# Performance work log

Hardware: AMD Instinct MI355X
Metric: run time of the kernel (lower is better)

## Reference

```python
import jax, jax.numpy as jnp
import numpy as np

D = 4096      # hidden_size
H = 32        # num_attention_heads
DH = 128      # head_dim
DR = 64       # rope_head_dim (rotated suffix of head_dim)
G = 4         # o_groups
QLR = 1536    # q_lora_rank
OLR = 512     # o_lora_rank
WIN = 2048    # window_size
EPS = 1e-6    # norm_eps
THETA = 10000.0


def rms_norm(x, g):
    return x * jax.lax.rsqrt(jnp.mean(x * x, axis=-1, keepdims=True) + EPS) * g


def rope_interleave(x, cos, sin):
    # interleaved (non-neox) rotary: pairs are adjacent even/odd lanes
    x0, x1 = x[..., 0::2], x[..., 1::2]
    r0 = x0 * cos - x1 * sin
    r1 = x0 * sin + x1 * cos
    return jnp.stack([r0, r1], axis=-1).reshape(x.shape)


def setup_inputs() -> dict:
    ks = jax.random.split(jax.random.key(0), 9)
    B, S = 1, 2048
    return {
        "hidden_states": jax.random.normal(ks[0], (B, S, D), jnp.float32),
        "positions": jnp.arange(S, dtype=jnp.int64),
        "wq_a": jax.random.normal(ks[1], (QLR, D), jnp.float32) * 0.02,
        "q_norm_g": jnp.ones((QLR,), jnp.float32),
        "wq_b": jax.random.normal(ks[2], (H * DH, QLR), jnp.float32) * 0.02,
        "wkv": jax.random.normal(ks[3], (DH, D), jnp.float32) * 0.02,
        "kv_norm_g": jnp.ones((DH,), jnp.float32),
        "wo_a": jax.random.normal(ks[4], (G, OLR, (H * DH) // G), jnp.float32) * 0.02,
        "wo_b": jax.random.normal(ks[5], (D, G * OLR), jnp.float32) * 0.02,
        "attn_sink": jax.random.normal(ks[6], (H,), jnp.float32),
    }


def reference(hidden_states, positions, wq_a, q_norm_g, wq_b, wkv, kv_norm_g, wo_a, wo_b, attn_sink):
    B, S, _ = hidden_states.shape
    # low-rank Q path: wq_a -> RMSNorm -> wq_b -> [B,S,H,DH]
    qr = rms_norm(hidden_states @ wq_a.T, q_norm_g)
    q = (qr @ wq_b.T).reshape(B, S, H, DH)
    # shared latent KV (single head_dim vector, MLA/MQA style): wkv -> RMSNorm
    kv = rms_norm(hidden_states @ wkv.T, kv_norm_g)  # [B,S,DH]
    # rotary tables (interleave mode)
    inv_freq = 1.0 / (THETA ** (jnp.arange(0, DR, 2, dtype=jnp.float32) / DR))
    ang = positions.astype(jnp.float32)[:, None] * inv_freq  # [S, DR/2]
    cos, sin = jnp.cos(ang), jnp.sin(ang)
    # rotate last DR dims of q and k
    q = jnp.concatenate(
        [q[..., : DH - DR], rope_interleave(q[..., DH - DR :], cos[None, :, None, :], sin[None, :, None, :])], -1)
    k = jnp.concatenate(
        [kv[..., : DH - DR], rope_interleave(kv[..., DH - DR :], cos[None, :, :], sin[None, :, :])], -1)
    # windowed causal attention with learned per-head sink logit
    scores = jnp.einsum("bshd,btd->bhst", q, k) * (DH ** -0.5)  # [B,H,S,S]
    i = jnp.arange(S)[:, None]
    j = jnp.arange(S)[None, :]
    mask = (j <= i) & ((i - j) < WIN)
    scores = jnp.where(mask[None, None], scores, jnp.finfo(scores.dtype).min)
    sink = jnp.broadcast_to(attn_sink[None, :, None, None], (B, H, S, 1))
    probs = jax.nn.softmax(jnp.concatenate([scores, sink], axis=-1), axis=-1)[..., :S]
    # value = shared normalized latent (pre-rope)
    out = jnp.einsum("bhst,btd->bshd", probs, kv)  # [B,S,H,DH]
    # grouped low-rank output projection: wo_a per group, then wo_b
    out = out.reshape(B, S, G, (H * DH) // G)
    low = jnp.einsum("bsgd,gkd->bsgk", out, wo_a).reshape(B, S, G * OLR)
    return low @ wo_b.T
```

## Files before the change

kernel.cpp:

```cpp
#include <hip/hip_runtime.h>

typedef unsigned short u16;
typedef __bf16 bf16x8 __attribute__((ext_vector_type(8)));
typedef float  f32x4  __attribute__((ext_vector_type(4)));

#define EPSF 1e-6f

__device__ __forceinline__ u16 f2b(float f) {
  unsigned u = __float_as_uint(f);
  u += 0x7fffu + ((u >> 16) & 1u);
  return (u16)(u >> 16);
}
__device__ __forceinline__ float b2f(u16 u) { return __uint_as_float(((unsigned)u) << 16); }
__device__ __forceinline__ u16 f2bh(float f) { return __builtin_bit_cast(u16, (__bf16)f); }

__device__ __forceinline__ void dma16(const u16* g, u16* l) {
  __builtin_amdgcn_global_load_lds(
      (const __attribute__((address_space(1))) unsigned int*)g,
      (__attribute__((address_space(3))) unsigned int*)l, 16, 0, 0);
}

__global__ void dsv4_cvt(const float* __restrict__ hidden, const float* __restrict__ wq_a,
                         const float* __restrict__ wq_b, const float* __restrict__ wkv,
                         const float* __restrict__ wo_a, const float* __restrict__ wo_b,
                         u16* hb, u16* qab, u16* qbb, u16* kvb, u16* oab, u16* obb)
{
  long c = (long)blockIdx.x * 256 + threadIdx.x;
  const float* s; u16* d; long off;
  if      (c < 1048576) { s = hidden; d = hb;  off = c; }
  else if (c < 1835008) { s = wq_a;   d = qab; off = c - 1048576; }
  else if (c < 2621440) { s = wq_b;   d = qbb; off = c - 1835008; }
  else if (c < 2686976) { s = wkv;    d = kvb; off = c - 2621440; }
  else if (c < 2949120) { s = wo_a;   d = oab; off = c - 2686976; }
  else                  { s = wo_b;   d = obb; off = c - 2949120; }
  const float* p = s + off * 8;
  float4 f0 = *(const float4*)p;
  float4 f1 = *(const float4*)(p + 4);
  union { u16 h[8]; int4 v; } u;
  u.h[0] = f2b(f0.x); u.h[1] = f2b(f0.y); u.h[2] = f2b(f0.z); u.h[3] = f2b(f0.w);
  u.h[4] = f2b(f1.x); u.h[5] = f2b(f1.y); u.h[6] = f2b(f1.z); u.h[7] = f2b(f1.w);
  *(int4*)(d + off * 8) = u.v;
}

template<int BM, bool C_F32>
__global__ __launch_bounds__(256, 2)
void dsv4_gemm(const u16* __restrict__ A, int lda, long sAz,
               const u16* __restrict__ B, int ldb, long sBz,
               void* __restrict__ Cv, int ldc, long sCz,
               int K, int splitTile,
               const u16* __restrict__ Baux, void* __restrict__ Caux, int ldcAux)
{
  constexpr int AI = (BM * 4) / 256;
  constexpr int NJ = (BM == 128) ? 4 : 2;
  __shared__ __align__(16) u16 As[BM * 32];
  __shared__ __align__(16) u16 Bs[128 * 32];

  const int tid   = threadIdx.x;
  const int lane  = tid & 63;
  const int q     = lane >> 4;
  const int l16   = lane & 15;
  const int wid   = tid >> 6;
  const int wbase = tid & 192;

  int n0 = blockIdx.x * 128;
  const int m0 = blockIdx.y * BM;
  void* Cp = Cv;
  if ((int)blockIdx.x >= splitTile) {
    B = Baux; Cp = Caux; ldc = ldcAux;
    n0 = ((int)blockIdx.x - splitTile) * 128;
  }
  A += (long)blockIdx.z * sAz;
  B += (long)blockIdx.z * sBz;

  const u16* gA[AI]; u16* lA[AI];
#pragma unroll
  for (int j = 0; j < AI; j++) {
    int L = j * 256 + tid, row = L >> 2, c = (L & 3) ^ ((row >> 1) & 3);
    gA[j] = A + (long)(m0 + row) * lda + c * 8;
    lA[j] = As + (j * 256 + wbase) * 8;
  }
  const u16* gB[2]; u16* lB[2];
#pragma unroll
  for (int j = 0; j < 2; j++) {
    int L = j * 256 + tid, row = L >> 2, c = (L & 3) ^ ((row >> 1) & 3);
    gB[j] = B + (long)(n0 + row) * ldb + c * 8;
    lB[j] = Bs + (j * 256 + wbase) * 8;
  }

  f32x4 acc[4][NJ];
#pragma unroll
  for (int i = 0; i < 4; i++)
#pragma unroll
    for (int j = 0; j < NJ; j++) { f32x4 z = {0.f, 0.f, 0.f, 0.f}; acc[i][j] = z; }

  const int wm = (BM == 128) ? (wid >> 1) * 64 : 0;
  const int wn = (BM == 128) ? (wid & 1) * 64 : wid * 32;

  for (int k0 = 0; k0 < K; k0 += 32) {
    __syncthreads();
#pragma unroll
    for (int j = 0; j < AI; j++) dma16(gA[j] + k0, lA[j]);
#pragma unroll
    for (int j = 0; j < 2; j++)  dma16(gB[j] + k0, lB[j]);
    asm volatile("s_waitcnt vmcnt(0)" ::: "memory");
    __syncthreads();

    bf16x8 af[4], bg[NJ];
#pragma unroll
    for (int i = 0; i < 4; i++) {
      int row = wm + i * 16 + l16;
      af[i] = *(const bf16x8*)&As[row * 32 + ((q ^ ((row >> 1) & 3)) << 3)];
    }
#pragma unroll
    for (int j = 0; j < NJ; j++) {
      int row = wn + j * 16 + l16;
      bg[j] = *(const bf16x8*)&Bs[row * 32 + ((q ^ ((row >> 1) & 3)) << 3)];
    }
#pragma unroll
    for (int i = 0; i < 4; i++)
#pragma unroll
      for (int j = 0; j < NJ; j++)
        acc[i][j] = __builtin_amdgcn_mfma_f32_16x16x32_bf16(af[i], bg[j], acc[i][j], 0, 0, 0);
  }

#pragma unroll
  for (int i = 0; i < 4; i++)
#pragma unroll
    for (int j = 0; j < NJ; j++)
#pragma unroll
      for (int rr = 0; rr < 4; rr++) {
        long row = m0 + wm + i * 16 + q * 4 + rr;
        int  col = n0 + wn + j * 16 + l16;
        if (C_F32)
          ((float*)Cp)[row * ldc + col + (long)blockIdx.z * sCz] = acc[i][j][rr];
        else
          ((u16*)Cp)[row * ldc + col + (long)blockIdx.z * sCz] = f2b(acc[i][j][rr]);
      }
}

__global__ void dsv4_rmsnorm(const u16* __restrict__ X, const float* __restrict__ g,
                             u16* __restrict__ Y, int W, float invW)
{
  __shared__ float wsum[4];
  const int row = blockIdx.x;
  const u16* x = X + (long)row * W;
  u16* y = Y + (long)row * W;
  float ss = 0.f;
  for (int i = threadIdx.x; i < W; i += 256) { float v = b2f(x[i]); ss += v * v; }
#pragma unroll
  for (int o = 32; o > 0; o >>= 1) ss += __shfl_xor(ss, o);
  const int wid = threadIdx.x >> 6;
  if ((threadIdx.x & 63) == 0) wsum[wid] = ss;
  __syncthreads();
  float tot = wsum[0] + wsum[1] + wsum[2] + wsum[3];
  float scale = rsqrtf(tot * invW + EPSF);
  for (int i = threadIdx.x; i < W; i += 256)
    y[i] = f2b(b2f(x[i]) * scale * g[i]);
}

__global__ void dsv4_kv_finalize(const u16* __restrict__ KVp, const float* __restrict__ g,
                                 u16* __restrict__ Kout, u16* __restrict__ VTout)
{
  const int wid  = threadIdx.x >> 6;
  const int lane = threadIdx.x & 63;
  const int row  = blockIdx.x * 4 + wid;
  const u16* x = KVp + (long)row * 128;
  float x0 = b2f(x[2 * lane]);
  float x1 = b2f(x[2 * lane + 1]);
  float ss = x0 * x0 + x1 * x1;
#pragma unroll
  for (int o = 32; o > 0; o >>= 1) ss += __shfl_xor(ss, o);
  float scale = rsqrtf(ss * (1.f / 128.f) + EPSF);
  float v0 = x0 * scale * g[2 * lane];
  float v1 = x1 * scale * g[2 * lane + 1];
  VTout[(long)(2 * lane) * 2048 + row]     = f2b(v0);
  VTout[(long)(2 * lane + 1) * 2048 + row] = f2b(v1);
  float k0 = v0, k1 = v1;
  if (lane >= 32) {
    int i = lane - 32;
    float invf = powf(10000.f, -(float)i * (1.f / 32.f));
    float sn, cc;
    sincosf((float)row * invf, &sn, &cc);
    k0 = v0 * cc - v1 * sn;
    k1 = v0 * sn + v1 * cc;
  }
  Kout[(long)row * 128 + 2 * lane]     = f2b(k0);
  Kout[(long)row * 128 + 2 * lane + 1] = f2b(k1);
}

__device__ __forceinline__ void attn_step(
    const bf16x8* qf, bool diag, const u16* __restrict__ KsB,
    const u16* __restrict__ VsB, u16* __restrict__ PsW,
    int w, int qd, int l16, int swz, float* m, float* negm, float* l, f32x4* o)
{
  const float scl2 = 0.12754245006257017f;
  const float THRU = 62.0f;
  f32x4 st[4];
#pragma unroll
  for (int i = 0; i < 4; i++) { f32x4 z = {0.f, 0.f, 0.f, 0.f}; st[i] = z; }

  __builtin_amdgcn_s_setprio(1);
#pragma unroll
  for (int ks = 0; ks < 4; ks++) {
#pragma unroll
    for (int nt = 0; nt < 4; nt++) {
      int row = nt * 16 + l16;
      bf16x8 bk = *(const bf16x8*)&KsB[row * 128 + ((((ks << 2) + qd) ^ swz) << 3)];
      st[nt] = __builtin_amdgcn_mfma_f32_16x16x32_bf16(qf[ks], bk, st[nt], 0, 0, 0);
    }
  }
  __builtin_amdgcn_s_setprio(0);

  if (diag) {
#pragma unroll
    for (int nt = 0; nt < 4; nt++)
#pragma unroll
      for (int rr = 0; rr < 4; rr++)
        if ((nt * 16 + l16) > (w * 16 + qd * 4 + rr)) st[nt][rr] = -3.0e38f;
  }

  float tm[4];
  bool need = false;
#pragma unroll
  for (int rr = 0; rr < 4; rr++) {
    float t = fmaxf(fmaxf(st[0][rr], st[1][rr]), fmaxf(st[2][rr], st[3][rr]));
    t = fmaxf(t, __shfl_xor(t, 1));
    t = fmaxf(t, __shfl_xor(t, 2));
    t = fmaxf(t, __shfl_xor(t, 4));
    t = fmaxf(t, __shfl_xor(t, 8));
    tm[rr] = t;
    need = need || (t > m[rr] + THRU);
  }
  if (__any(need)) {
#pragma unroll
    for (int rr = 0; rr < 4; rr++) {
      float mn = fmaxf(m[rr], tm[rr]);
      float a  = exp2f(scl2 * (m[rr] - mn));
      m[rr] = mn; negm[rr] = -scl2 * mn;
      l[rr] *= a;
#pragma unroll
      for (int nt = 0; nt < 8; nt++) o[nt][rr] *= a;
    }
  }

#pragma unroll
  for (int nt = 0; nt < 4; nt++)
#pragma unroll
    for (int rr = 0; rr < 4; rr++) {
      float p = exp2f(fmaf(st[nt][rr], scl2, negm[rr]));
      l[rr] += p;
      int row = qd * 4 + rr;
      int cl2 = ((nt << 1) + (l16 >> 3)) ^ (row & 7);
      PsW[row * 64 + (cl2 << 3) + (l16 & 7)] = f2bh(p);
    }
  asm volatile("s_waitcnt lgkmcnt(0)" ::: "memory");

  __builtin_amdgcn_s_setprio(1);
#pragma unroll
  for (int ks = 0; ks < 2; ks++) {
    bf16x8 ap = *(const bf16x8*)&PsW[l16 * 64 + ((((ks << 2) + qd) ^ swz) << 3)];
#pragma unroll
    for (int nt = 0; nt < 8; nt++) {
      int row = nt * 16 + l16;
      bf16x8 bv = *(const bf16x8*)&VsB[row * 64 + ((((ks << 2) + qd) ^ swz) << 3)];
      o[nt] = __builtin_amdgcn_mfma_f32_16x16x32_bf16(ap, bv, o[nt], 0, 0, 0);
    }
  }
  __builtin_amdgcn_s_setprio(0);
}

__global__ __launch_bounds__(256, 2)
void dsv4_attn(const u16* __restrict__ Q, const u16* __restrict__ Km,
               const u16* __restrict__ VT, const float* __restrict__ sinkp,
               u16* __restrict__ O)
{
  __shared__ __align__(16) u16 Ks[2][64 * 128];
  __shared__ __align__(16) u16 Vs[2][128 * 64];
  __shared__ __align__(16) u16 Ps[4][16 * 64];

  const int b  = blockIdx.x;
  const int h  = blockIdx.y;
  const int qtA = 31 - b, qtB = b;
  const int n1 = qtA + 1, nT = n1 + qtB + 1;
  const int tid  = threadIdx.x;
  const int lane = tid & 63;
  const int w    = tid >> 6;
  const int qd   = lane >> 4;
  const int l16  = lane & 15;
  const int swz  = l16 & 7;

  bf16x8 qfA[4], qfB[4];
#pragma unroll
  for (int t = 0; t < 2; t++) {
    int srow = (t ? qtB : qtA) * 64 + w * 16 + l16;
    const u16* qp = Q + (long)srow * 4096 + h * 128 + qd * 8;
    bf16x8* qf = t ? qfB : qfA;
#pragma unroll
    for (int ks = 0; ks < 4; ks++) {
      union { int4 v; u16 hh[8]; } u;
      u.v = *(const int4*)(qp + ks * 32);
      if (ks >= 2) {
#pragma unroll
        for (int j = 0; j < 4; j++) {
          int i = (ks - 2) * 16 + qd * 4 + j;
          float invf = exp2f((float)i * (-13.287712379549449f / 32.f));
          float sn, cc;
          sincosf((float)srow * invf, &sn, &cc);
          float x0 = b2f(u.hh[2 * j]), x1 = b2f(u.hh[2 * j + 1]);
          u.hh[2 * j]     = f2b(x0 * cc - x1 * sn);
          u.hh[2 * j + 1] = f2b(x0 * sn + x1 * cc);
        }
      }
      qf[ks] = *(bf16x8*)&u;
    }
  }

  const u16* gK[4]; const u16* gV[4]; int lKo[4], lVo[4];
#pragma unroll
  for (int j = 0; j < 4; j++) {
    int cl = j * 256 + tid;
    int krow = cl >> 4, kc = (cl & 15) ^ (krow & 7);
    gK[j] = Km + (long)krow * 128 + kc * 8;
    lKo[j] = (j * 256 + (tid & 192)) * 8;
    int vrow = cl >> 3, vc = (cl & 7) ^ (vrow & 7);
    gV[j] = VT + (long)vrow * 2048 + vc * 8;
    lVo[j] = (j * 256 + (tid & 192)) * 8;
  }

  float m[4], negm[4], l[4];
  f32x4 o[8];
#pragma unroll
  for (int i = 0; i < 4; i++) { m[i] = -INFINITY; negm[i] = 0.f; l[i] = 0.f; }
#pragma unroll
  for (int i = 0; i < 8; i++) { f32x4 z = {0.f, 0.f, 0.f, 0.f}; o[i] = z; }

  const float sink2 = sinkp[h] * 1.4426950408889634f;

#pragma unroll
  for (int j = 0; j < 4; j++) { dma16(gK[j], &Ks[0][lKo[j]]); dma16(gV[j], &Vs[0][lVo[j]]); }

  for (int it = 0; it < nT; ++it) {
    int nxt = it + 1;
    if (nxt < nT) {
      int kt2 = (nxt < n1) ? nxt : nxt - n1;
      int pb = nxt & 1;
#pragma unroll
      for (int j = 0; j < 4; j++) {
        dma16(gK[j] + (long)kt2 * 8192, &Ks[pb][lKo[j]]);
        dma16(gV[j] + (long)kt2 * 64,   &Vs[pb][lVo[j]]);
      }
    }
    asm volatile("s_waitcnt vmcnt(8)" ::: "memory");
    asm volatile("s_barrier" ::: "memory");
    const int cb = it & 1;

    if (it < n1)
      attn_step(qfA, it == n1 - 1, Ks[cb], Vs[cb], Ps[w], w, qd, l16, swz, m, negm, l, o);
    else
      attn_step(qfB, it == nT - 1, Ks[cb], Vs[cb], Ps[w], w, qd, l16, swz, m, negm, l, o);

    asm volatile("s_barrier" ::: "memory");

    if (it == n1 - 1) {
      float inv[4];
#pragma unroll
      for (int rr = 0; rr < 4; rr++) {
        float ls = l[rr];
        ls += __shfl_xor(ls, 1);
        ls += __shfl_xor(ls, 2);
        ls += __shfl_xor(ls, 4);
        ls += __shfl_xor(ls, 8);
        inv[rr] = 1.f / (ls + exp2f(sink2 + negm[rr]));
      }
#pragma unroll
      for (int nt = 0; nt < 8; nt++)
#pragma unroll
        for (int rr = 0; rr < 4; rr++)
          O[(long)(qtA * 64 + w * 16 + qd * 4 + rr) * 4096 + h * 128 + nt * 16 + l16] =
              f2bh(o[nt][rr] * inv[rr]);
#pragma unroll
      for (int i = 0; i < 4; i++) { m[i] = -INFINITY; negm[i] = 0.f; l[i] = 0.f; }
#pragma unroll
      for (int i = 0; i < 8; i++) { f32x4 z = {0.f, 0.f, 0.f, 0.f}; o[i] = z; }
    }
  }

  float inv[4];
#pragma unroll
  for (int rr = 0; rr < 4; rr++) {
    float ls = l[rr];
    ls += __shfl_xor(ls, 1);
    ls += __shfl_xor(ls, 2);
    ls += __shfl_xor(ls, 4);
    ls += __shfl_xor(ls, 8);
    inv[rr] = 1.f / (ls + exp2f(sink2 + negm[rr]));
  }
#pragma unroll
  for (int nt = 0; nt < 8; nt++)
#pragma unroll
    for (int rr = 0; rr < 4; rr++)
      O[(long)(qtB * 64 + w * 16 + qd * 4 + rr) * 4096 + h * 128 + nt * 16 + l16] =
          f2bh(o[nt][rr] * inv[rr]);
}

extern "C" void kernel_launch(void* const* d_in, const int* in_sizes, int n_in,
                              void* d_out, int out_size, void* d_ws, size_t ws_size,
                              hipStream_t stream)
{
  (void)in_sizes; (void)n_in; (void)out_size; (void)ws_size;
  const float* hidden = (const float*)d_in[0];
  const float* wq_a  = (const float*)d_in[2];
  const float* q_g   = (const float*)d_in[3];
  const float* wq_b  = (const float*)d_in[4];
  const float* wkv   = (const float*)d_in[5];
  const float* kv_g  = (const float*)d_in[6];
  const float* wo_a  = (const float*)d_in[7];
  const float* wo_b  = (const float*)d_in[8];
  const float* sinkp = (const float*)d_in[9];
  float* out = (float*)d_out;

  char* ws = (char*)d_ws;
  u16* hb     = (u16*)(ws);
  u16* low    = (u16*)(ws);
  u16* qab    = (u16*)(ws + (17ul << 20));
  u16* qr     = (u16*)(ws + (17ul << 20));
  u16* qbb    = (u16*)(ws + (30ul << 20));
  u16* kvb    = (u16*)(ws + (43ul << 20));
  u16* oab    = (u16*)(ws + (45ul << 20));
  u16* obb    = (u16*)(ws + (50ul << 20));
  u16* qbuf   = (u16*)(ws + (67ul << 20));
  u16* attnout= (u16*)(ws + (84ul << 20));
  u16* qr_pre = (u16*)(ws + (101ul << 20));
  u16* kvpre  = (u16*)(ws + (108ul << 20));
  u16* kmat   = (u16*)(ws + (108ul << 20) + 524288u);
  u16* vt     = (u16*)(ws + (108ul << 20) + 1048576u);

  const int BIG = 1 << 29;
  dim3 blk(256);

  dsv4_cvt<<<15616, blk, 0, stream>>>(hidden, wq_a, wq_b, wkv, wo_a, wo_b,
                                      hb, qab, qbb, kvb, oab, obb);
  dsv4_gemm<64, false><<<dim3(13, 32, 1), blk, 0, stream>>>(
      hb, 4096, 0, qab, 4096, 0, qr_pre, 1536, 0, 4096, 12, kvb, kvpre, 128);
  dsv4_rmsnorm<<<2048, blk, 0, stream>>>(qr_pre, q_g, qr, 1536, 1.f / 1536.f);
  dsv4_kv_finalize<<<512, blk, 0, stream>>>(kvpre, kv_g, kmat, vt);
  dsv4_gemm<128, false><<<dim3(32, 16, 1), blk, 0, stream>>>(
      qr, 1536, 0, qbb, 1536, 0, qbuf, 4096, 0, 1536, BIG, nullptr, nullptr, 0);
  dsv4_attn<<<dim3(16, 32, 1), blk, 0, stream>>>(qbuf, kmat, vt, sinkp, attnout);
  dsv4_gemm<64, false><<<dim3(4, 32, 4), blk, 0, stream>>>(
      attnout, 4096, 1024, oab, 1024, 524288, low, 2048, 512, 1024, BIG,
      nullptr, nullptr, 0);
  dsv4_gemm<128, true><<<dim3(32, 16, 1), blk, 0, stream>>>(
      low, 2048, 0, obb, 2048, 0, out, 4096, 0, 2048, BIG, nullptr, nullptr, 0);
}
```

Measured before the change: 440.8 us.

## Double-buffer GEMM LDS tiles to overlap global loads with MFMA

The GEMM kernel's LDS A/B tiles become two buffers. The next K-slice's global-to-LDS DMA is issued right after the barrier, while MFMAs run on the current slice, instead of waiting for each load before computing. This aims to hide global memory latency, at the cost of twice the shared memory. With one barrier per step, a wave that is still reading the old buffer may race the DMA that overwrites it, since the LDS reads are not fenced before the next iteration's DMA. Occupancy may also fall.

Result: no change. 434.8 us (-1.4%).

```diff
diff --git a/kernel.cpp b/kernel.cpp
--- a/kernel.cpp
+++ b/kernel.cpp
@@ -52,8 +52,8 @@
 {
   constexpr int AI = (BM * 4) / 256;
   constexpr int NJ = (BM == 128) ? 4 : 2;
-  __shared__ __align__(16) u16 As[BM * 32];
-  __shared__ __align__(16) u16 Bs[128 * 32];
+  __shared__ __align__(16) u16 As[2 * BM * 32];
+  __shared__ __align__(16) u16 Bs[2 * 128 * 32];
 
   const int tid   = threadIdx.x;
   const int lane  = tid & 63;
@@ -96,25 +96,39 @@
   const int wm = (BM == 128) ? (wid >> 1) * 64 : 0;
   const int wn = (BM == 128) ? (wid & 1) * 64 : wid * 32;
 
-  for (int k0 = 0; k0 < K; k0 += 32) {
-    __syncthreads();
-#pragma unroll
-    for (int j = 0; j < AI; j++) dma16(gA[j] + k0, lA[j]);
-#pragma unroll
-    for (int j = 0; j < 2; j++)  dma16(gB[j] + k0, lB[j]);
+#pragma unroll
+  for (int j = 0; j < AI; j++) dma16(gA[j], lA[j]);
+#pragma unroll
+  for (int j = 0; j < 2; j++)  dma16(gB[j], lB[j]);
+
+  const int nsteps = K >> 5;
+  for (int t = 0; t < nsteps; t++) {
     asm volatile("s_waitcnt vmcnt(0)" ::: "memory");
-    __syncthreads();
+    __builtin_amdgcn_s_barrier();
+    const int cur = t & 1;
+    const int aoff = cur * (BM * 32);
+    const int boff = cur * (128 * 32);
+
+    if (t + 1 < nsteps) {
+      const int k = (t + 1) << 5;
+      const int na = (cur ^ 1) * (BM * 32);
+      const int nb = (cur ^ 1) * (128 * 32);
+#pragma unroll
+      for (int j = 0; j < AI; j++) dma16(gA[j] + k, lA[j] + na);
+#pragma unroll
+      for (int j = 0; j < 2; j++)  dma16(gB[j] + k, lB[j] + nb);
+    }
 
     bf16x8 af[4], bg[NJ];
 #pragma unroll
     for (int i = 0; i < 4; i++) {
       int row = wm + i * 16 + l16;
-      af[i] = *(const bf16x8*)&As[row * 32 + ((q ^ ((row >> 1) & 3)) << 3)];
+      af[i] = *(const bf16x8*)&As[aoff + row * 32 + ((q ^ ((row >> 1) & 3)) << 3)];
     }
 #pragma unroll
     for (int j = 0; j < NJ; j++) {
       int row = wn + j * 16 + l16;
-      bg[j] = *(const bf16x8*)&Bs[row * 32 + ((q ^ ((row >> 1) & 3)) << 3)];
+      bg[j] = *(const bf16x8*)&Bs[boff + row * 32 + ((q ^ ((row >> 1) & 3)) << 3)];
     }
 #pragma unroll
     for (int i = 0; i < 4; i++)
```

## Double-buffer GEMM LDS tiles with K=64 steps and async prefetch

Applied to the files above, without the earlier changes.

Restructures the bf16 GEMM main loop to use two LDS buffers, each holding a 64-wide K slice. The next slice is issued via global_load_lds before computing on the current one, and there is one barrier per step instead of two syncthreads. The swizzle is widened to 8 chunks per row, and setprio is raised around the MFMA blocks. This aims to overlap global loads with MFMA work and cut barrier overhead, at the cost of four times the LDS per block, which may reduce occupancy.

After: 403.1 us. 8.6% less time.

```diff
diff --git a/kernel.cpp b/kernel.cpp
--- a/kernel.cpp
+++ b/kernel.cpp
@@ -50,17 +50,18 @@
                int K, int splitTile,
                const u16* __restrict__ Baux, void* __restrict__ Caux, int ldcAux)
 {
-  constexpr int AI = (BM * 4) / 256;
+  constexpr int AJ = BM / 32;
   constexpr int NJ = (BM == 128) ? 4 : 2;
-  __shared__ __align__(16) u16 As[BM * 32];
-  __shared__ __align__(16) u16 Bs[128 * 32];
+  __shared__ __align__(16) u16 As[2 * BM * 64];
+  __shared__ __align__(16) u16 Bs[2 * 128 * 64];
 
   const int tid   = threadIdx.x;
   const int lane  = tid & 63;
-  const int q     = lane >> 4;
+  const int qd    = lane >> 4;
   const int l16   = lane & 15;
   const int wid   = tid >> 6;
   const int wbase = tid & 192;
+  const int swz   = l16 & 7;
 
   int n0 = blockIdx.x * 128;
   const int m0 = blockIdx.y * BM;
@@ -72,17 +73,17 @@
   A += (long)blockIdx.z * sAz;
   B += (long)blockIdx.z * sBz;
 
-  const u16* gA[AI]; u16* lA[AI];
-#pragma unroll
-  for (int j = 0; j < AI; j++) {
-    int L = j * 256 + tid, row = L >> 2, c = (L & 3) ^ ((row >> 1) & 3);
+  const u16* gA[AJ]; u16* lA[AJ];
+#pragma unroll
+  for (int j = 0; j < AJ; j++) {
+    int L = j * 256 + tid, row = L >> 3, c = (L & 7) ^ (row & 7);
     gA[j] = A + (long)(m0 + row) * lda + c * 8;
     lA[j] = As + (j * 256 + wbase) * 8;
   }
-  const u16* gB[2]; u16* lB[2];
-#pragma unroll
-  for (int j = 0; j < 2; j++) {
-    int L = j * 256 + tid, row = L >> 2, c = (L & 3) ^ ((row >> 1) & 3);
+  const u16* gB[4]; u16* lB[4];
+#pragma unroll
+  for (int j = 0; j < 4; j++) {
+    int L = j * 256 + tid, row = L >> 3, c = (L & 7) ^ (row & 7);
     gB[j] = B + (long)(n0 + row) * ldb + c * 8;
     lB[j] = Bs + (j * 256 + wbase) * 8;
   }
@@ -96,31 +97,51 @@
   const int wm = (BM == 128) ? (wid >> 1) * 64 : 0;
   const int wn = (BM == 128) ? (wid & 1) * 64 : wid * 32;
 
-  for (int k0 = 0; k0 < K; k0 += 32) {
-    __syncthreads();
-#pragma unroll
-    for (int j = 0; j < AI; j++) dma16(gA[j] + k0, lA[j]);
-#pragma unroll
-    for (int j = 0; j < 2; j++)  dma16(gB[j] + k0, lB[j]);
+  auto issue = [&](int s) {
+    const int k  = s << 6;
+    const int ab = (s & 1) * (BM * 64);
+    const int bb = (s & 1) * (128 * 64);
+#pragma unroll
+    for (int j = 0; j < AJ; j++) dma16(gA[j] + k, lA[j] + ab);
+#pragma unroll
+    for (int j = 0; j < 4; j++)  dma16(gB[j] + k, lB[j] + bb);
+  };
+
+  const int nsteps = K >> 6;
+  issue(0);
+  asm volatile("s_waitcnt vmcnt(0)" ::: "memory");
+  __builtin_amdgcn_s_barrier();
+
+  for (int t = 0; t < nsteps; t++) {
+    if (t + 1 < nsteps) issue(t + 1);
+    const int ab = (t & 1) * (BM * 64);
+    const int bb = (t & 1) * (128 * 64);
+
+#pragma unroll
+    for (int ks2 = 0; ks2 < 2; ks2++) {
+      bf16x8 af[4], bg[NJ];
+#pragma unroll
+      for (int i = 0; i < 4; i++) {
+        int row = wm + i * 16 + l16;
+        af[i] = *(const bf16x8*)&As[ab + row * 64 + ((((ks2 << 2) + qd) ^ swz) << 3)];
+      }
+#pragma unroll
+      for (int j = 0; j < NJ; j++) {
+        int row = wn + j * 16 + l16;
+        bg[j] = *(const bf16x8*)&Bs[bb + row * 64 + ((((ks2 << 2) + qd) ^ swz) << 3)];
+      }
+      __builtin_amdgcn_s_setprio(1);
+#pragma unroll
+      for (int i = 0; i < 4; i++)
+#pragma unroll
+        for (int j = 0; j < NJ; j++)
+          acc[i][j] = __builtin_amdgcn_mfma_f32_16x16x32_bf16(af[i], bg[j], acc[i][j], 0, 0, 0);
+      __builtin_amdgcn_s_setprio(0);
+    }
+
+    asm volatile("s_waitcnt lgkmcnt(0)" ::: "memory");
     asm volatile("s_waitcnt vmcnt(0)" ::: "memory");
-    __syncthreads();
-
-    bf16x8 af[4], bg[NJ];
-#pragma unroll
-    for (int i = 0; i < 4; i++) {
-      int row = wm + i * 16 + l16;
-      af[i] = *(const bf16x8*)&As[row * 32 + ((q ^ ((row >> 1) & 3)) << 3)];
-    }
-#pragma unroll
-    for (int j = 0; j < NJ; j++) {
-      int row = wn + j * 16 + l16;
-      bg[j] = *(const bf16x8*)&Bs[row * 32 + ((q ^ ((row >> 1) & 3)) << 3)];
-    }
-#pragma unroll
-    for (int i = 0; i < 4; i++)
-#pragma unroll
-      for (int j = 0; j < NJ; j++)
-        acc[i][j] = __builtin_amdgcn_mfma_f32_16x16x32_bf16(af[i], bg[j], acc[i][j], 0, 0, 0);
+    __builtin_amdgcn_s_barrier();
   }
 
 #pragma unroll
@@ -129,7 +150,7 @@
     for (int j = 0; j < NJ; j++)
 #pragma unroll
       for (int rr = 0; rr < 4; rr++) {
-        long row = m0 + wm + i * 16 + q * 4 + rr;
+        long row = m0 + wm + i * 16 + qd * 4 + rr;
         int  col = n0 + wn + j * 16 + l16;
         if (C_F32)
           ((float*)Cp)[row * ldc + col + (long)blockIdx.z * sCz] = acc[i][j][rr];
```
